# Kernel optimization log

Measured on AMD Instinct MI355X. Metric: run time of the kernel, lower is better.

## Reference

```python
import jax, jax.numpy as jnp
import numpy as np

GH, GW = 16, 16          # group_size
DIM = 512
H = 8                    # num_heads
PD = DIM // 16           # pos_dim = (dim//4)//4 = 32
B = 256                  # number of groups (batch*windows)
N = GH * GW


def _make_bias_tables():
    # biases buffer: all 2D relative offsets, shape [(2GH-1)*(2GW-1), 2]
    h = np.arange(1 - GH, GH)
    w = np.arange(1 - GW, GW)
    bh, bw = np.meshgrid(h, w, indexing='ij')
    biases = np.stack([bh, bw]).reshape(2, -1).T.astype(np.float32)
    # relative_position_index: [N, N] lookup into the bias table
    ch, cw = np.meshgrid(np.arange(GH), np.arange(GW), indexing='ij')
    coords = np.stack([ch, cw]).reshape(2, -1)            # [2, N]
    rel = coords[:, :, None] - coords[:, None, :]         # [2, N, N]
    rel = rel.transpose(1, 2, 0).copy()                   # [N, N, 2]
    rel[:, :, 0] += GH - 1
    rel[:, :, 1] += GW - 1
    rel[:, :, 0] *= 2 * GW - 1
    idx = rel.sum(-1)
    return biases, idx.astype(np.int32)


def _ln(x, g, b, eps=1e-5):
    m = x.mean(-1, keepdims=True)
    v = ((x - m) ** 2).mean(-1, keepdims=True)
    return (x - m) / jnp.sqrt(v + eps) * g + b


def setup_inputs() -> dict:
    key = jax.random.key(0)
    ks = jax.random.split(key, 16)
    s = 0.02
    biases_np, idx_np = _make_bias_tables()
    return {
        'x': jax.random.normal(ks[0], (B, N, DIM), dtype=jnp.float32),
        'qkv_w': jax.random.normal(ks[1], (DIM, 3 * DIM), dtype=jnp.float32) * s,
        'qkv_b': jnp.zeros((3 * DIM,), jnp.float32),
        'proj_w': jax.random.normal(ks[2], (DIM, DIM), dtype=jnp.float32) * s,
        'proj_b': jnp.zeros((DIM,), jnp.float32),
        'p1_w': jax.random.normal(ks[3], (2, PD), dtype=jnp.float32) * s,
        'p1_b': jnp.zeros((PD,), jnp.float32),
        'g1': jnp.ones((PD,), jnp.float32), 'b1': jnp.zeros((PD,), jnp.float32),
        'p2_w': jax.random.normal(ks[4], (PD, PD), dtype=jnp.float32) * s,
        'p2_b': jnp.zeros((PD,), jnp.float32),
        'g2': jnp.ones((PD,), jnp.float32), 'b2': jnp.zeros((PD,), jnp.float32),
        'p3_w': jax.random.normal(ks[5], (PD, PD), dtype=jnp.float32) * s,
        'p3_b': jnp.zeros((PD,), jnp.float32),
        'g3': jnp.ones((PD,), jnp.float32), 'b3': jnp.zeros((PD,), jnp.float32),
        'p4_w': jax.random.normal(ks[6], (PD, H), dtype=jnp.float32) * s,
        'p4_b': jnp.zeros((H,), jnp.float32),
        'biases': jnp.asarray(biases_np),
        'rel_idx': jnp.asarray(idx_np),
    }


def reference(x, qkv_w, qkv_b, proj_w, proj_b,
              p1_w, p1_b, g1, b1, p2_w, p2_b, g2, b2,
              p3_w, p3_b, g3, b3, p4_w, p4_b, biases, rel_idx):
    Bn, Nn, C = x.shape
    hd = C // H
    scale = hd ** -0.5
    qkv = (x @ qkv_w + qkv_b).reshape(Bn, Nn, 3, H, hd).transpose(2, 0, 3, 1, 4)
    q, k, v = qkv[0] * scale, qkv[1], qkv[2]      # [B, H, N, hd]
    attn = jnp.einsum('bhnd,bhmd->bhnm', q, k)    # [B, H, N, N]
    # dynamic position bias MLP on the offset table
    h1 = jax.nn.relu(_ln(biases @ p1_w + p1_b, g1, b1))
    h2 = jax.nn.relu(_ln(h1 @ p2_w + p2_b, g2, b2))
    h3 = jax.nn.relu(_ln(h2 @ p3_w + p3_b, g3, b3))
    pos = h3 @ p4_w + p4_b                        # [L, H]
    rpb = pos[rel_idx.reshape(-1)].reshape(Nn, Nn, H).transpose(2, 0, 1)  # [H, N, N]
    attn = jax.nn.softmax(attn + rpb[None], axis=-1)
    out = jnp.einsum('bhnm,bhmd->bhnd', attn, v)
    out = out.transpose(0, 2, 1, 3).reshape(Bn, Nn, C)
    return out @ proj_w + proj_b
```

## Files before the change

### kernel.cpp

```cpp
#include <hip/hip_runtime.h>
#include <stdint.h>

typedef __bf16 bf16x8 __attribute__((ext_vector_type(8)));
typedef float  f32x4  __attribute__((ext_vector_type(4)));
typedef unsigned short ushort_t;

#define MFMA16(a,b,c) __builtin_amdgcn_mfma_f32_16x16x32_bf16((a),(b),(c),0,0,0)

#define GLOAD16(gsrc, ldst) \
    __builtin_amdgcn_global_load_lds((const __attribute__((address_space(1))) void*)(gsrc), \
                                     (__attribute__((address_space(3))) void*)(ldst), 16, 0, 0)

#define BATCH 256
#define NTOK  256
#define DIM   512
#define NH    8
#define HD    64
#define PD    32
#define LTAB  961

#define POS_OFF   0
#define RPB_OFF   32768
#define WQKV_OFF  (RPB_OFF + 2097152)
#define WPROJ_OFF (WQKV_OFF + 1572864)
#define QKV_OFF   (WPROJ_OFF + 524288)
#define AOUT_OFF  (QKV_OFF + 201326592)
#define XB_OFF    AOUT_OFF

__device__ __forceinline__ ushort_t f2bf(float f) {
    unsigned int u = __builtin_bit_cast(unsigned int, f);
    u += 0x7FFFu + ((u >> 16) & 1u);
    return (ushort_t)(u >> 16);
}

__global__ __launch_bounds__(256) void convert_x(
    const float* __restrict__ x, ushort_t* __restrict__ xb)
{
    size_t i = ((size_t)blockIdx.x * 256 + threadIdx.x) * 8;
    float4 f0 = *(const float4*)(x + i);
    float4 f1 = *(const float4*)(x + i + 4);
    uint4 o;
    o.x = (unsigned)f2bf(f0.x) | ((unsigned)f2bf(f0.y) << 16);
    o.y = (unsigned)f2bf(f0.z) | ((unsigned)f2bf(f0.w) << 16);
    o.z = (unsigned)f2bf(f1.x) | ((unsigned)f2bf(f1.y) << 16);
    o.w = (unsigned)f2bf(f1.z) | ((unsigned)f2bf(f1.w) << 16);
    *reinterpret_cast<uint4*>(xb + i) = o;
}

__global__ __launch_bounds__(256) void transpose_w(
    const float* __restrict__ src, ushort_t* __restrict__ dst, int K, int Nn)
{
    __shared__ ushort_t tile[64][65];
    int tiles_n = Nn >> 6;
    int tn = blockIdx.x % tiles_n, tk = blockIdx.x / tiles_n;
    int n0 = tn * 64, k0 = tk * 64;
    int t = threadIdx.x;
#pragma unroll
    for (int i = 0; i < 16; i++) {
        int idx = t + i * 256;
        int kl = idx >> 6, nl = idx & 63;
        tile[nl][kl] = f2bf(src[(size_t)(k0 + kl) * Nn + n0 + nl]);
    }
    __syncthreads();
#pragma unroll
    for (int i = 0; i < 16; i++) {
        int idx = t + i * 256;
        int nl = idx >> 6, kl = idx & 63;
        dst[(size_t)(n0 + nl) * K + k0 + kl] = tile[nl][kl];
    }
}

__device__ __forceinline__ float ln_relu_t(float h, int j,
                                           const float* __restrict__ g,
                                           const float* __restrict__ bb) {
    float m = h;
    m += __shfl_xor(m, 1); m += __shfl_xor(m, 2); m += __shfl_xor(m, 4);
    m += __shfl_xor(m, 8); m += __shfl_xor(m, 16);
    m *= (1.0f / PD);
    float d = h - m;
    float v = d * d;
    v += __shfl_xor(v, 1); v += __shfl_xor(v, 2); v += __shfl_xor(v, 4);
    v += __shfl_xor(v, 8); v += __shfl_xor(v, 16);
    v *= (1.0f / PD);
    float x = d * rsqrtf(v + 1e-5f) * g[j] + bb[j];
    return x > 0.f ? x : 0.f;
}

__global__ __launch_bounds__(256) void pos_mlp(
    const float* __restrict__ biases,
    const float* __restrict__ p1_w, const float* __restrict__ p1_b,
    const float* __restrict__ g1, const float* __restrict__ b1,
    const float* __restrict__ p2_w, const float* __restrict__ p2_b,
    const float* __restrict__ g2, const float* __restrict__ b2,
    const float* __restrict__ p3_w, const float* __restrict__ p3_b,
    const float* __restrict__ g3, const float* __restrict__ b3,
    const float* __restrict__ p4_w, const float* __restrict__ p4_b,
    float* __restrict__ pos)
{
    __shared__ float hs[8][33];
    int tid = threadIdx.x;
    int rl = tid >> 5, j = tid & 31;
    int r = blockIdx.x * 8 + rl;
    bool ok = r < LTAB;
    float c0 = ok ? biases[r * 2 + 0] : 0.f;
    float c1 = ok ? biases[r * 2 + 1] : 0.f;

    float h = c0 * p1_w[j] + c1 * p1_w[PD + j] + p1_b[j];
    h = ln_relu_t(h, j, g1, b1);

    hs[rl][j] = h;
    __syncthreads();
    float s = p2_b[j];
#pragma unroll
    for (int i = 0; i < PD; i++) s += hs[rl][i] * p2_w[i * PD + j];
    __syncthreads();
    h = ln_relu_t(s, j, g2, b2);

    hs[rl][j] = h;
    __syncthreads();
    s = p3_b[j];
#pragma unroll
    for (int i = 0; i < PD; i++) s += hs[rl][i] * p3_w[i * PD + j];
    __syncthreads();
    h = ln_relu_t(s, j, g3, b3);

    hs[rl][j] = h;
    __syncthreads();
    if (ok && j < NH) {
        float o = p4_b[j];
#pragma unroll
        for (int i = 0; i < PD; i++) o += hs[rl][i] * p4_w[i * NH + j];
        pos[r * NH + j] = o;
    }
}

__global__ __launch_bounds__(256) void rpb_gather(
    const float* __restrict__ pos, const int* __restrict__ rel_idx,
    float* __restrict__ rpb)
{
    int i = blockIdx.x * 256 + threadIdx.x;
    int idx = rel_idx[i];
#pragma unroll
    for (int hh = 0; hh < NH; hh++) rpb[(size_t)hh * 65536 + i] = pos[idx * NH + hh];
}

__global__ __launch_bounds__(256) void qkv_gemm(
    const ushort_t* __restrict__ xb, const ushort_t* __restrict__ wT,
    const float* __restrict__ qkv_b, ushort_t* __restrict__ qkvb)
{
    __shared__ ushort_t As[3][4096];
    __shared__ ushort_t Bs[3][4096];
    int t = threadIdx.x;
    int bid = blockIdx.x;
    int wgid = (bid & 7) * 768 + (bid >> 3);
    int mt = wgid / 12, nt = wgid % 12;
    int m0 = mt * 128, n0 = nt * 128;
    int lane = t & 63, w = t >> 6;
    int wm = w >> 1, wn = w & 1;
    int lr = lane & 15, lk = lane >> 4;
    int srow = lane >> 2;
    int scol = (((lane & 3) ^ ((lane >> 3) & 3)) << 3);
    const ushort_t* Asrc = xb + (size_t)(m0 + srow) * 512 + scol;
    const ushort_t* Bsrc = wT + (size_t)(n0 + srow) * 512 + scol;
    int rx = ((lk ^ ((lr >> 1) & 3)) << 3);

    f32x4 acc[4][4];
#pragma unroll
    for (int fr = 0; fr < 4; fr++)
#pragma unroll
        for (int fc = 0; fc < 4; fc++) acc[fr][fc] = (f32x4){0.f, 0.f, 0.f, 0.f};

#define QSTAGE(buf, kt) do { \
    _Pragma("unroll") \
    for (int i_ = 0; i_ < 2; i_++) { \
        int row_ = w * 32 + i_ * 16; \
        GLOAD16(Asrc + (size_t)row_ * 512 + (kt) * 32, &As[buf][row_ * 32]); \
        GLOAD16(Bsrc + (size_t)row_ * 512 + (kt) * 32, &Bs[buf][row_ * 32]); \
    } } while (0)

    QSTAGE(0, 0);
    QSTAGE(1, 1);
    asm volatile("s_waitcnt vmcnt(4)" ::: "memory");
    __syncthreads();
#pragma unroll
    for (int kt = 0; kt < 16; ++kt) {
        int cb = kt % 3;
        if (kt + 2 < 16) QSTAGE((kt + 2) % 3, kt + 2);
        bf16x8 a[4], b[4];
#pragma unroll
        for (int fr = 0; fr < 4; fr++)
            a[fr] = *reinterpret_cast<const bf16x8*>(&As[cb][(wm * 64 + fr * 16 + lr) * 32 + rx]);
#pragma unroll
        for (int fc = 0; fc < 4; fc++)
            b[fc] = *reinterpret_cast<const bf16x8*>(&Bs[cb][(wn * 64 + fc * 16 + lr) * 32 + rx]);
#pragma unroll
        for (int fr = 0; fr < 4; fr++)
#pragma unroll
            for (int fc = 0; fc < 4; fc++)
                acc[fr][fc] = MFMA16(a[fr], b[fc], acc[fr][fc]);
        if (kt + 2 < 16) {
            asm volatile("s_waitcnt vmcnt(4)" ::: "memory");
            __syncthreads();
        } else if (kt + 1 < 16) {
            asm volatile("s_waitcnt vmcnt(0)" ::: "memory");
            __syncthreads();
        }
    }
#undef QSTAGE

    int s = n0 >> 9;
    if (s < 2) {
        float sc = (s == 0) ? 0.125f : 1.0f;
#pragma unroll
        for (int fc = 0; fc < 4; fc++) {
            int n = n0 + wn * 64 + fc * 16 + lr;
            float bias = qkv_b[n];
            int hh = (n >> 6) & 7, d = n & 63;
#pragma unroll
            for (int fr = 0; fr < 4; fr++)
#pragma unroll
                for (int r = 0; r < 4; r++) {
                    int m = m0 + wm * 64 + fr * 16 + lk * 4 + r;
                    int bg = m >> 8, tok = m & 255;
                    float v = (acc[fr][fc][r] + bias) * sc;
                    qkvb[((((size_t)s * 256 + bg) * 8 + hh) * 256 + tok) * 64 + d] = f2bf(v);
                }
        }
    } else {
#pragma unroll
        for (int fc = 0; fc < 4; fc++) {
            int n = n0 + wn * 64 + fc * 16 + lr;
            float bias = qkv_b[n];
            int hh = (n >> 6) & 7, d = n & 63;
#pragma unroll
            for (int fr = 0; fr < 4; fr++) {
                int m = m0 + wm * 64 + fr * 16 + lk * 4;
                int bg = m >> 8, tok = m & 255;
                uint2 pk;
                pk.x = (unsigned)f2bf(acc[fr][fc][0] + bias) |
                       ((unsigned)f2bf(acc[fr][fc][1] + bias) << 16);
                pk.y = (unsigned)f2bf(acc[fr][fc][2] + bias) |
                       ((unsigned)f2bf(acc[fr][fc][3] + bias) << 16);
                *reinterpret_cast<uint2*>(
                    qkvb + ((((size_t)512 + bg) * 8 + hh) * 64 + d) * 256 + tok) = pk;
            }
        }
    }
}

__global__ __launch_bounds__(256) void attn_kernel(
    const ushort_t* __restrict__ qkvb, const float* __restrict__ rpb,
    ushort_t* __restrict__ aout)
{
    __shared__ ushort_t Ps[4][32][40];
    __shared__ ushort_t Os[4][16 * 72];
    int t = threadIdx.x, lane = t & 63, w = t >> 6;
    int bid = blockIdx.x;
    int qh = bid & 1; int bh = bid >> 1; int hh = bh & 7; int bg = bh >> 3;
    const ushort_t* Qg  = qkvb + (((size_t)bg * 8 + hh) * 256) * 64;
    const ushort_t* Kg  = qkvb + (((size_t)(256 + bg) * 8 + hh) * 256) * 64;
    const ushort_t* VTg = qkvb + (((size_t)(512 + bg) * 8 + hh) * 64) * 256;
    int lr = lane & 15, lk = lane >> 4;
    int qrow0 = qh * 128 + w * 32;

    bf16x8 qf[2][2];
#pragma unroll
    for (int fr = 0; fr < 2; fr++)
#pragma unroll
        for (int kc = 0; kc < 2; kc++)
            qf[fr][kc] = *reinterpret_cast<const bf16x8*>(
                Qg + (size_t)(qrow0 + fr * 16 + lr) * 64 + kc * 32 + lk * 8);

    f32x4 oacc[2][4];
    float rsum[2][4];
#pragma unroll
    for (int fr = 0; fr < 2; fr++) {
#pragma unroll
        for (int fc = 0; fc < 4; fc++) oacc[fr][fc] = (f32x4){0.f, 0.f, 0.f, 0.f};
#pragma unroll
        for (int r = 0; r < 4; r++) rsum[fr][r] = 0.f;
    }

    for (int kt = 0; kt < 8; ++kt) {
        f32x4 sacc[2][2];
#pragma unroll
        for (int fr = 0; fr < 2; fr++)
#pragma unroll
            for (int fc = 0; fc < 2; fc++) sacc[fr][fc] = (f32x4){0.f, 0.f, 0.f, 0.f};
#pragma unroll
        for (int kc = 0; kc < 2; kc++) {
            bf16x8 kb0 = *reinterpret_cast<const bf16x8*>(
                Kg + (size_t)(kt * 32 + lr) * 64 + kc * 32 + lk * 8);
            bf16x8 kb1 = *reinterpret_cast<const bf16x8*>(
                Kg + (size_t)(kt * 32 + 16 + lr) * 64 + kc * 32 + lk * 8);
            sacc[0][0] = MFMA16(qf[0][kc], kb0, sacc[0][0]);
            sacc[0][1] = MFMA16(qf[0][kc], kb1, sacc[0][1]);
            sacc[1][0] = MFMA16(qf[1][kc], kb0, sacc[1][0]);
            sacc[1][1] = MFMA16(qf[1][kc], kb1, sacc[1][1]);
        }
#pragma unroll
        for (int fr = 0; fr < 2; fr++)
#pragma unroll
            for (int fc = 0; fc < 2; fc++)
#pragma unroll
                for (int r = 0; r < 4; r++) {
                    int row = qrow0 + fr * 16 + lk * 4 + r;
                    int col = kt * 32 + fc * 16 + lr;
                    float lg = sacc[fr][fc][r] + rpb[((size_t)hh * 256 + row) * 256 + col];
                    float p = __expf(lg);
                    rsum[fr][r] += p;
                    Ps[w][fr * 16 + lk * 4 + r][fc * 16 + lr] = f2bf(p);
                }
        bf16x8 pa[2], vb[4];
#pragma unroll
        for (int fr = 0; fr < 2; fr++)
            pa[fr] = *reinterpret_cast<const bf16x8*>(&Ps[w][fr * 16 + lr][lk * 8]);
#pragma unroll
        for (int fc = 0; fc < 4; fc++)
            vb[fc] = *reinterpret_cast<const bf16x8*>(
                VTg + (size_t)(fc * 16 + lr) * 256 + kt * 32 + lk * 8);
#pragma unroll
        for (int fr = 0; fr < 2; fr++)
#pragma unroll
            for (int fc = 0; fc < 4; fc++)
                oacc[fr][fc] = MFMA16(pa[fr], vb[fc], oacc[fr][fc]);
    }
    float rinv[2][4];
#pragma unroll
    for (int fr = 0; fr < 2; fr++)
#pragma unroll
        for (int r = 0; r < 4; r++) {
            float s = rsum[fr][r];
            s += __shfl_xor(s, 1); s += __shfl_xor(s, 2);
            s += __shfl_xor(s, 4); s += __shfl_xor(s, 8);
            rinv[fr][r] = __frcp_rn(s);
        }
#pragma unroll
    for (int fr = 0; fr < 2; fr++) {
#pragma unroll
        for (int fc = 0; fc < 4; fc++)
#pragma unroll
            for (int r = 0; r < 4; r++)
                Os[w][(lk * 4 + r) * 72 + fc * 16 + lr] = f2bf(oacc[fr][fc][r] * rinv[fr][r]);
#pragma unroll
        for (int ii = 0; ii < 2; ii++) {
            int j = lane + ii * 64;
            int row = j >> 3, ch = j & 7;
            uint4 v = *reinterpret_cast<const uint4*>(&Os[w][row * 72 + ch * 8]);
            *reinterpret_cast<uint4*>(
                aout + ((size_t)(bg * 256 + qrow0 + fr * 16 + row)) * 512 + hh * 64 + ch * 8) = v;
        }
    }
}

__global__ __launch_bounds__(256) void proj_gemm(
    const ushort_t* __restrict__ ain, const ushort_t* __restrict__ wT,
    const float* __restrict__ proj_b, float* __restrict__ out)
{
    __shared__ ushort_t As[3][4096];
    __shared__ ushort_t Bs[3][4096];
    int t = threadIdx.x;
    int bid = blockIdx.x;
    int wgid = (bid & 7) * 256 + (bid >> 3);
    int mt = wgid / 4, nt = wgid % 4;
    int m0 = mt * 128, n0 = nt * 128;
    int lane = t & 63, w = t >> 6;
    int wm = w >> 1, wn = w & 1;
    int lr = lane & 15, lk = lane >> 4;
    int srow = lane >> 2;
    int scol = (((lane & 3) ^ ((lane >> 3) & 3)) << 3);
    const ushort_t* Asrc = ain + (size_t)(m0 + srow) * 512 + scol;
    const ushort_t* Bsrc = wT + (size_t)(n0 + srow) * 512 + scol;
    int rx = ((lk ^ ((lr >> 1) & 3)) << 3);
    f32x4 acc[4][4];
#pragma unroll
    for (int fr = 0; fr < 4; fr++)
#pragma unroll
        for (int fc = 0; fc < 4; fc++) acc[fr][fc] = (f32x4){0.f, 0.f, 0.f, 0.f};

#define PSTAGE(buf, kt) do { \
    _Pragma("unroll") \
    for (int i_ = 0; i_ < 2; i_++) { \
        int row_ = w * 32 + i_ * 16; \
        GLOAD16(Asrc + (size_t)row_ * 512 + (kt) * 32, &As[buf][row_ * 32]); \
        GLOAD16(Bsrc + (size_t)row_ * 512 + (kt) * 32, &Bs[buf][row_ * 32]); \
    } } while (0)

    PSTAGE(0, 0);
    PSTAGE(1, 1);
    asm volatile("s_waitcnt vmcnt(4)" ::: "memory");
    __syncthreads();
#pragma unroll
    for (int kt = 0; kt < 16; ++kt) {
        int cb = kt % 3;
        if (kt + 2 < 16) PSTAGE((kt + 2) % 3, kt + 2);
        bf16x8 a[4], b[4];
#pragma unroll
        for (int fr = 0; fr < 4; fr++)
            a[fr] = *reinterpret_cast<const bf16x8*>(&As[cb][(wm * 64 + fr * 16 + lr) * 32 + rx]);
#pragma unroll
        for (int fc = 0; fc < 4; fc++)
            b[fc] = *reinterpret_cast<const bf16x8*>(&Bs[cb][(wn * 64 + fc * 16 + lr) * 32 + rx]);
#pragma unroll
        for (int fr = 0; fr < 4; fr++)
#pragma unroll
            for (int fc = 0; fc < 4; fc++)
                acc[fr][fc] = MFMA16(a[fr], b[fc], acc[fr][fc]);
        if (kt + 2 < 16) {
            asm volatile("s_waitcnt vmcnt(4)" ::: "memory");
            __syncthreads();
        } else if (kt + 1 < 16) {
            asm volatile("s_waitcnt vmcnt(0)" ::: "memory");
            __syncthreads();
        }
    }
#undef PSTAGE
#pragma unroll
    for (int fc = 0; fc < 4; fc++) {
        int n = n0 + wn * 64 + fc * 16 + lr;
        float bias = proj_b[n];
#pragma unroll
        for (int fr = 0; fr < 4; fr++)
#pragma unroll
            for (int r = 0; r < 4; r++) {
                int m = m0 + wm * 64 + fr * 16 + lk * 4 + r;
                out[(size_t)m * 512 + n] = acc[fr][fc][r] + bias;
            }
    }
}

extern "C" void kernel_launch(void* const* d_in, const int* in_sizes, int n_in,
                              void* d_out, int out_size, void* d_ws, size_t ws_size,
                              hipStream_t stream) {
    const float* x      = (const float*)d_in[0];
    const float* qkv_w  = (const float*)d_in[1];
    const float* qkv_b  = (const float*)d_in[2];
    const float* proj_w = (const float*)d_in[3];
    const float* proj_b = (const float*)d_in[4];
    const float* p1_w = (const float*)d_in[5];
    const float* p1_b = (const float*)d_in[6];
    const float* g1   = (const float*)d_in[7];
    const float* b1   = (const float*)d_in[8];
    const float* p2_w = (const float*)d_in[9];
    const float* p2_b = (const float*)d_in[10];
    const float* g2   = (const float*)d_in[11];
    const float* b2   = (const float*)d_in[12];
    const float* p3_w = (const float*)d_in[13];
    const float* p3_b = (const float*)d_in[14];
    const float* g3   = (const float*)d_in[15];
    const float* b3   = (const float*)d_in[16];
    const float* p4_w = (const float*)d_in[17];
    const float* p4_b = (const float*)d_in[18];
    const float* biases  = (const float*)d_in[19];
    const int*   rel_idx = (const int*)d_in[20];
    float* out = (float*)d_out;

    char* ws = (char*)d_ws;
    float*    pos    = (float*)(ws + POS_OFF);
    float*    rpb    = (float*)(ws + RPB_OFF);
    ushort_t* wqkvT  = (ushort_t*)(ws + WQKV_OFF);
    ushort_t* wprojT = (ushort_t*)(ws + WPROJ_OFF);
    ushort_t* qkvb   = (ushort_t*)(ws + QKV_OFF);
    ushort_t* aoutb  = (ushort_t*)(ws + AOUT_OFF);
    ushort_t* xb     = (ushort_t*)(ws + XB_OFF);

    convert_x<<<dim3(16384), dim3(256), 0, stream>>>(x, xb);
    transpose_w<<<dim3(24 * 8), dim3(256), 0, stream>>>(qkv_w, wqkvT, 512, 1536);
    transpose_w<<<dim3(8 * 8), dim3(256), 0, stream>>>(proj_w, wprojT, 512, 512);
    pos_mlp<<<dim3(121), dim3(256), 0, stream>>>(biases, p1_w, p1_b, g1, b1,
                                                 p2_w, p2_b, g2, b2,
                                                 p3_w, p3_b, g3, b3,
                                                 p4_w, p4_b, pos);
    rpb_gather<<<dim3(256), dim3(256), 0, stream>>>(pos, rel_idx, rpb);
    qkv_gemm<<<dim3(512 * 12), dim3(256), 0, stream>>>(xb, wqkvT, qkv_b, qkvb);
    attn_kernel<<<dim3(4096), dim3(256), 0, stream>>>(qkvb, rpb, aoutb);
    proj_gemm<<<dim3(512 * 4), dim3(256), 0, stream>>>(aoutb, wprojT, proj_b, out);
}
```

Measured before the change: 429.9 us.

## Enlarge QKV and projection GEMM tiles to 256x256 with 512-thread blocks

Both GEMMs move from 128x128 tiles with 4 waves and a 3-stage K=32 pipeline to 256x256 tiles with 8 waves, a 2-stage double buffer and K=64 steps. Half the waves load A and the other half load B, using a new 8-chunk XOR swizzle, and each wave computes a 128x64 sub-tile. The aim is to raise arithmetic intensity and cut global and LDS traffic per FLOP. In exchange it uses 128 KB of LDS at one block per CU, waits for all loads with vmcnt(0) each step (weaker overlap), and needs many more accumulator registers.

```diff
diff --git a/kernel.cpp b/kernel.cpp
--- a/kernel.cpp
+++ b/kernel.cpp
@@ -144,64 +144,74 @@
     for (int hh = 0; hh < NH; hh++) rpb[(size_t)hh * 65536 + i] = pos[idx * NH + hh];
 }
 
-__global__ __launch_bounds__(256) void qkv_gemm(
+__global__ __launch_bounds__(512, 1) void qkv_gemm(
     const ushort_t* __restrict__ xb, const ushort_t* __restrict__ wT,
     const float* __restrict__ qkv_b, ushort_t* __restrict__ qkvb)
 {
-    __shared__ ushort_t As[3][4096];
-    __shared__ ushort_t Bs[3][4096];
+    __shared__ ushort_t As[2][256 * 64];
+    __shared__ ushort_t Bs[2][256 * 64];
     int t = threadIdx.x;
     int bid = blockIdx.x;
-    int wgid = (bid & 7) * 768 + (bid >> 3);
-    int mt = wgid / 12, nt = wgid % 12;
-    int m0 = mt * 128, n0 = nt * 128;
+    int wgid = (bid & 7) * 192 + (bid >> 3);
+    int mt = wgid / 6, nt = wgid % 6;
+    int m0 = mt * 256, n0 = nt * 256;
     int lane = t & 63, w = t >> 6;
-    int wm = w >> 1, wn = w & 1;
+    int wm = w >> 2, wn = w & 3;
     int lr = lane & 15, lk = lane >> 4;
-    int srow = lane >> 2;
-    int scol = (((lane & 3) ^ ((lane >> 3) & 3)) << 3);
-    const ushort_t* Asrc = xb + (size_t)(m0 + srow) * 512 + scol;
-    const ushort_t* Bsrc = wT + (size_t)(n0 + srow) * 512 + scol;
-    int rx = ((lk ^ ((lr >> 1) & 3)) << 3);
-
-    f32x4 acc[4][4];
-#pragma unroll
-    for (int fr = 0; fr < 4; fr++)
+    int srow8 = lane >> 3;
+    int sch = ((lane & 7) ^ srow8) * 8;
+    const ushort_t* Asrc = xb + (size_t)(m0 + srow8) * 512 + sch;
+    const ushort_t* Bsrc = wT + (size_t)(n0 + srow8) * 512 + sch;
+    int arw = w & 3;
+    int ch0 = ((lk) ^ (lr & 7)) * 8;
+    int ch1 = ((4 + lk) ^ (lr & 7)) * 8;
+    int arow = wm * 128 + lr;
+    int brow = wn * 64 + lr;
+
+    f32x4 acc[8][4];
+#pragma unroll
+    for (int fr = 0; fr < 8; fr++)
 #pragma unroll
         for (int fc = 0; fc < 4; fc++) acc[fr][fc] = (f32x4){0.f, 0.f, 0.f, 0.f};
 
 #define QSTAGE(buf, kt) do { \
-    _Pragma("unroll") \
-    for (int i_ = 0; i_ < 2; i_++) { \
-        int row_ = w * 32 + i_ * 16; \
-        GLOAD16(Asrc + (size_t)row_ * 512 + (kt) * 32, &As[buf][row_ * 32]); \
-        GLOAD16(Bsrc + (size_t)row_ * 512 + (kt) * 32, &Bs[buf][row_ * 32]); \
+    if (w < 4) { \
+        _Pragma("unroll") \
+        for (int i_ = 0; i_ < 8; i_++) { \
+            int rb_ = arw * 64 + i_ * 8; \
+            GLOAD16(Asrc + (size_t)rb_ * 512 + (kt) * 64, &As[buf][rb_ * 64]); \
+        } \
+    } else { \
+        _Pragma("unroll") \
+        for (int i_ = 0; i_ < 8; i_++) { \
+            int rb_ = arw * 64 + i_ * 8; \
+            GLOAD16(Bsrc + (size_t)rb_ * 512 + (kt) * 64, &Bs[buf][rb_ * 64]); \
+        } \
     } } while (0)
 
     QSTAGE(0, 0);
-    QSTAGE(1, 1);
-    asm volatile("s_waitcnt vmcnt(4)" ::: "memory");
-    __syncthreads();
-#pragma unroll
-    for (int kt = 0; kt < 16; ++kt) {
-        int cb = kt % 3;
-        if (kt + 2 < 16) QSTAGE((kt + 2) % 3, kt + 2);
-        bf16x8 a[4], b[4];
-#pragma unroll
-        for (int fr = 0; fr < 4; fr++)
-            a[fr] = *reinterpret_cast<const bf16x8*>(&As[cb][(wm * 64 + fr * 16 + lr) * 32 + rx]);
-#pragma unroll
-        for (int fc = 0; fc < 4; fc++)
-            b[fc] = *reinterpret_cast<const bf16x8*>(&Bs[cb][(wn * 64 + fc * 16 + lr) * 32 + rx]);
-#pragma unroll
-        for (int fr = 0; fr < 4; fr++)
+    asm volatile("s_waitcnt vmcnt(0)" ::: "memory");
+    __syncthreads();
+    for (int kt = 0; kt < 8; ++kt) {
+        int cb = kt & 1;
+        if (kt < 7) QSTAGE(cb ^ 1, kt + 1);
+#pragma unroll
+        for (int kh = 0; kh < 2; kh++) {
+            int ch = kh ? ch1 : ch0;
+            bf16x8 a[8], b[4];
+#pragma unroll
+            for (int fr = 0; fr < 8; fr++)
+                a[fr] = *reinterpret_cast<const bf16x8*>(&As[cb][(arow + fr * 16) * 64 + ch]);
 #pragma unroll
             for (int fc = 0; fc < 4; fc++)
-                acc[fr][fc] = MFMA16(a[fr], b[fc], acc[fr][fc]);
-        if (kt + 2 < 16) {
-            asm volatile("s_waitcnt vmcnt(4)" ::: "memory");
-            __syncthreads();
-        } else if (kt + 1 < 16) {
+                b[fc] = *reinterpret_cast<const bf16x8*>(&Bs[cb][(brow + fc * 16) * 64 + ch]);
+#pragma unroll
+            for (int fr = 0; fr < 8; fr++)
+#pragma unroll
+                for (int fc = 0; fc < 4; fc++)
+                    acc[fr][fc] = MFMA16(a[fr], b[fc], acc[fr][fc]);
+        }
+        if (kt < 7) {
             asm volatile("s_waitcnt vmcnt(0)" ::: "memory");
             __syncthreads();
         }
@@ -209,6 +219,7 @@
 #undef QSTAGE
 
     int s = n0 >> 9;
+    int bg = m0 >> 8;
     if (s < 2) {
         float sc = (s == 0) ? 0.125f : 1.0f;
 #pragma unroll
@@ -216,14 +227,13 @@
             int n = n0 + wn * 64 + fc * 16 + lr;
             float bias = qkv_b[n];
             int hh = (n >> 6) & 7, d = n & 63;
-#pragma unroll
-            for (int fr = 0; fr < 4; fr++)
+            ushort_t* dst = qkvb + ((((size_t)s * 256 + bg) * 8 + hh) * 256) * 64 + d;
+#pragma unroll
+            for (int fr = 0; fr < 8; fr++)
 #pragma unroll
                 for (int r = 0; r < 4; r++) {
-                    int m = m0 + wm * 64 + fr * 16 + lk * 4 + r;
-                    int bg = m >> 8, tok = m & 255;
-                    float v = (acc[fr][fc][r] + bias) * sc;
-                    qkvb[((((size_t)s * 256 + bg) * 8 + hh) * 256 + tok) * 64 + d] = f2bf(v);
+                    int tok = wm * 128 + fr * 16 + lk * 4 + r;
+                    dst[(size_t)tok * 64] = f2bf((acc[fr][fc][r] + bias) * sc);
                 }
         }
     } else {
@@ -232,17 +242,16 @@
             int n = n0 + wn * 64 + fc * 16 + lr;
             float bias = qkv_b[n];
             int hh = (n >> 6) & 7, d = n & 63;
-#pragma unroll
-            for (int fr = 0; fr < 4; fr++) {
-                int m = m0 + wm * 64 + fr * 16 + lk * 4;
-                int bg = m >> 8, tok = m & 255;
+            ushort_t* dst = qkvb + ((((size_t)512 + bg) * 8 + hh) * 64 + d) * 256;
+#pragma unroll
+            for (int fr = 0; fr < 8; fr++) {
+                int tok = wm * 128 + fr * 16 + lk * 4;
                 uint2 pk;
                 pk.x = (unsigned)f2bf(acc[fr][fc][0] + bias) |
                        ((unsigned)f2bf(acc[fr][fc][1] + bias) << 16);
                 pk.y = (unsigned)f2bf(acc[fr][fc][2] + bias) |
                        ((unsigned)f2bf(acc[fr][fc][3] + bias) << 16);
-                *reinterpret_cast<uint2*>(
-                    qkvb + ((((size_t)512 + bg) * 8 + hh) * 64 + d) * 256 + tok) = pk;
+                *reinterpret_cast<uint2*>(dst + tok) = pk;
             }
         }
     }
@@ -353,63 +362,74 @@
     }
 }
 
-__global__ __launch_bounds__(256) void proj_gemm(
+__global__ __launch_bounds__(512, 1) void proj_gemm(
     const ushort_t* __restrict__ ain, const ushort_t* __restrict__ wT,
     const float* __restrict__ proj_b, float* __restrict__ out)
 {
-    __shared__ ushort_t As[3][4096];
-    __shared__ ushort_t Bs[3][4096];
+    __shared__ ushort_t As[2][256 * 64];
+    __shared__ ushort_t Bs[2][256 * 64];
     int t = threadIdx.x;
     int bid = blockIdx.x;
-    int wgid = (bid & 7) * 256 + (bid >> 3);
-    int mt = wgid / 4, nt = wgid % 4;
-    int m0 = mt * 128, n0 = nt * 128;
+    int wgid = (bid & 7) * 64 + (bid >> 3);
+    int mt = wgid / 2, nt = wgid % 2;
+    int m0 = mt * 256, n0 = nt * 256;
     int lane = t & 63, w = t >> 6;
-    int wm = w >> 1, wn = w & 1;
+    int wm = w >> 2, wn = w & 3;
     int lr = lane & 15, lk = lane >> 4;
-    int srow = lane >> 2;
-    int scol = (((lane & 3) ^ ((lane >> 3) & 3)) << 3);
-    const ushort_t* Asrc = ain + (size_t)(m0 + srow) * 512 + scol;
-    const ushort_t* Bsrc = wT + (size_t)(n0 + srow) * 512 + scol;
-    int rx = ((lk ^ ((lr >> 1) & 3)) << 3);
-    f32x4 acc[4][4];
-#pragma unroll
-    for (int fr = 0; fr < 4; fr++)
+    int srow8 = lane >> 3;
+    int sch = ((lane & 7) ^ srow8) * 8;
+    const ushort_t* Asrc = ain + (size_t)(m0 + srow8) * 512 + sch;
+    const ushort_t* Bsrc = wT + (size_t)(n0 + srow8) * 512 + sch;
+    int arw = w & 3;
+    int ch0 = ((lk) ^ (lr & 7)) * 8;
+    int ch1 = ((4 + lk) ^ (lr & 7)) * 8;
+    int arow = wm * 128 + lr;
+    int brow = wn * 64 + lr;
+
+    f32x4 acc[8][4];
+#pragma unroll
+    for (int fr = 0; fr < 8; fr++)
 #pragma unroll
         for (int fc = 0; fc < 4; fc++) acc[fr][fc] = (f32x4){0.f, 0.f, 0.f, 0.f};
 
 #define PSTAGE(buf, kt) do { \
-    _Pragma("unroll") \
-    for (int i_ = 0; i_ < 2; i_++) { \
-        int row_ = w * 32 + i_ * 16; \
-        GLOAD16(Asrc + (size_t)row_ * 512 + (kt) * 32, &As[buf][row_ * 32]); \
-        GLOAD16(Bsrc + (size_t)row_ * 512 + (kt) * 32, &Bs[buf][row_ * 32]); \
+    if (w < 4) { \
+        _Pragma("unroll") \
+        for (int i_ = 0; i_ < 8; i_++) { \
+            int rb_ = arw * 64 + i_ * 8; \
+            GLOAD16(Asrc + (size_t)rb_ * 512 + (kt) * 64, &As[buf][rb_ * 64]); \
+        } \
+    } else { \
+        _Pragma("unroll") \
+        for (int i_ = 0; i_ < 8; i_++) { \
+            int rb_ = arw * 64 + i_ * 8; \
+            GLOAD16(Bsrc + (size_t)rb_ * 512 + (kt) * 64, &Bs[buf][rb_ * 64]); \
+        } \
     } } while (0)
 
     PSTAGE(0, 0);
-    PSTAGE(1, 1);
-    asm volatile("s_waitcnt vmcnt(4)" ::: "memory");
-    __syncthreads();
-#pragma unroll
-    for (int kt = 0; kt < 16; ++kt) {
-        int cb = kt % 3;
-        if (kt + 2 < 16) PSTAGE((kt + 2) % 3, kt + 2);
-        bf16x8 a[4], b[4];
-#pragma unroll
-        for (int fr = 0; fr < 4; fr++)
-            a[fr] = *reinterpret_cast<const bf16x8*>(&As[cb][(wm * 64 + fr * 16 + lr) * 32 + rx]);
-#pragma unroll
-        for (int fc = 0; fc < 4; fc++)
-            b[fc] = *reinterpret_cast<const bf16x8*>(&Bs[cb][(wn * 64 + fc * 16 + lr) * 32 + rx]);
-#pragma unroll
-        for (int fr = 0; fr < 4; fr++)
+    asm volatile("s_waitcnt vmcnt(0)" ::: "memory");
+    __syncthreads();
+    for (int kt = 0; kt < 8; ++kt) {
+        int cb = kt & 1;
+        if (kt < 7) PSTAGE(cb ^ 1, kt + 1);
+#pragma unroll
+        for (int kh = 0; kh < 2; kh++) {
+            int ch = kh ? ch1 : ch0;
+            bf16x8 a[8], b[4];
+#pragma unroll
+            for (int fr = 0; fr < 8; fr++)
+                a[fr] = *reinterpret_cast<const bf16x8*>(&As[cb][(arow + fr * 16) * 64 + ch]);
 #pragma unroll
             for (int fc = 0; fc < 4; fc++)
-                acc[fr][fc] = MFMA16(a[fr], b[fc], acc[fr][fc]);
-        if (kt + 2 < 16) {
-            asm volatile("s_waitcnt vmcnt(4)" ::: "memory");
-            __syncthreads();
-        } else if (kt + 1 < 16) {
+                b[fc] = *reinterpret_cast<const bf16x8*>(&Bs[cb][(brow + fc * 16) * 64 + ch]);
+#pragma unroll
+            for (int fr = 0; fr < 8; fr++)
+#pragma unroll
+                for (int fc = 0; fc < 4; fc++)
+                    acc[fr][fc] = MFMA16(a[fr], b[fc], acc[fr][fc]);
+        }
+        if (kt < 7) {
             asm volatile("s_waitcnt vmcnt(0)" ::: "memory");
             __syncthreads();
         }
@@ -420,10 +440,10 @@
         int n = n0 + wn * 64 + fc * 16 + lr;
         float bias = proj_b[n];
 #pragma unroll
-        for (int fr = 0; fr < 4; fr++)
+        for (int fr = 0; fr < 8; fr++)
 #pragma unroll
             for (int r = 0; r < 4; r++) {
-                int m = m0 + wm * 64 + fr * 16 + lk * 4 + r;
+                int m = m0 + wm * 128 + fr * 16 + lk * 4 + r;
                 out[(size_t)m * 512 + n] = acc[fr][fc][r] + bias;
             }
     }
@@ -472,7 +492,7 @@
                                                  p3_w, p3_b, g3, b3,
                                                  p4_w, p4_b, pos);
     rpb_gather<<<dim3(256), dim3(256), 0, stream>>>(pos, rel_idx, rpb);
-    qkv_gemm<<<dim3(512 * 12), dim3(256), 0, stream>>>(xb, wqkvT, qkv_b, qkvb);
+    qkv_gemm<<<dim3(1536), dim3(512), 0, stream>>>(xb, wqkvT, qkv_b, qkvb);
     attn_kernel<<<dim3(4096), dim3(256), 0, stream>>>(qkvb, rpb, aoutb);
-    proj_gemm<<<dim3(512 * 4), dim3(256), 0, stream>>>(aoutb, wprojT, proj_b, out);
-}
+    proj_gemm<<<dim3(512), dim3(512), 0, stream>>>(aoutb, wprojT, proj_b, out);
+}
```

After: 383.0 us. 10.9% less time.
